# Performance work log

Hardware: AMD Instinct MI355X
Metric: run time of the kernel (lower is better)

## Reference

```python
import jax, jax.numpy as jnp
import numpy as np

B, NQ, C = 2, 16384, 768
NH, NL, NP = 6, 1, 4
HW = 128
D = C // NH  # 128, deform_ratio = 1.0
EPS = 1e-6


def layernorm(x, g, b):
    m = jnp.mean(x, -1, keepdims=True)
    v = jnp.var(x, -1, keepdims=True)
    return (x - m) * jax.lax.rsqrt(v + EPS) * g + b


def setup_inputs() -> dict:
    key = jax.random.key(0)
    ks = jax.random.split(key, 16)
    n = lambda k, s, sc=1.0: jax.random.normal(k, s, jnp.float32) * sc
    return {
        "query": n(ks[0], (B, NQ, C)),
        "reference_points": jax.random.uniform(ks[1], (B, NQ, NL, 2), jnp.float32),
        "feat": n(ks[2], (B, NQ, C)),
        "spatial_shapes": jnp.array([[HW, HW]], jnp.int32),
        "level_start_index": jnp.array([0], jnp.int32),
        "qn_g": jnp.ones((C,), jnp.float32), "qn_b": jnp.zeros((C,), jnp.float32),
        "fn_g": jnp.ones((C,), jnp.float32), "fn_b": jnp.zeros((C,), jnp.float32),
        "gamma": n(ks[3], (C,), 0.1),
        "W_off": n(ks[4], (C, NH * NL * NP * 2), 0.02), "b_off": n(ks[5], (NH * NL * NP * 2,), 0.5),
        "W_attn": n(ks[6], (C, NH * NL * NP), 0.02), "b_attn": jnp.zeros((NH * NL * NP,), jnp.float32),
        "W_val": n(ks[7], (C, NH * D), 0.02), "b_val": jnp.zeros((NH * D,), jnp.float32),
        "W_out": n(ks[8], (NH * D, C), 0.02), "b_out": jnp.zeros((C,), jnp.float32),
    }


def _ms_deform_attn(q, rp, f, W_off, b_off, W_attn, b_attn, W_val, b_val, W_out, b_out, shapes, starts):
    Bq, Nq, _ = q.shape
    value = (f @ W_val + b_val).reshape(Bq, -1, NH, D)  # (B, Lin, H, D)
    off = (q @ W_off + b_off).reshape(Bq, Nq, NH, NL, NP, 2)
    aw = jax.nn.softmax((q @ W_attn + b_attn).reshape(Bq, Nq, NH, NL * NP), -1)
    aw = aw.reshape(Bq, Nq, NH, NL, NP)
    shapes_f = jnp.asarray(shapes, q.dtype)
    normalizer = jnp.stack([shapes_f[:, 1], shapes_f[:, 0]], -1)  # (NL, 2) = (W, H)
    loc = rp[:, :, None, :, None, :] + off / normalizer[None, None, None, :, None, :]
    out = jnp.zeros((Bq, Nq, NH, D), q.dtype)
    b_idx = jnp.arange(Bq)[:, None, None, None]
    h_idx = jnp.arange(NH)[None, None, :, None]
    for l in range(NL):
        Hl, Wl = int(shapes[l, 0]), int(shapes[l, 1])
        s = int(starts[l])
        v = value[:, s:s + Hl * Wl].reshape(Bq, Hl, Wl, NH, D)
        ll = loc[:, :, :, l]                        # (B, Nq, H, P, 2)
        # grid_sample bilinear, align_corners=False, zero padding
        x = ll[..., 0] * Wl - 0.5
        y = ll[..., 1] * Hl - 0.5
        x0 = jnp.floor(x); y0 = jnp.floor(y)
        x1 = x0 + 1.0;     y1 = y0 + 1.0
        wx1 = x - x0; wx0 = 1.0 - wx1
        wy1 = y - y0; wy0 = 1.0 - wy1
        def corner(xi, yi, w):
            valid = (xi >= 0) & (xi <= Wl - 1) & (yi >= 0) & (yi <= Hl - 1)
            xc = jnp.clip(xi, 0, Wl - 1).astype(jnp.int32)
            yc = jnp.clip(yi, 0, Hl - 1).astype(jnp.int32)
            g = v[b_idx, yc, xc, h_idx]             # (B, Nq, H, P, D)
            return g * (w * valid)[..., None]
        samp = (corner(x0, y0, wx0 * wy0) + corner(x1, y0, wx1 * wy0)
                + corner(x0, y1, wx0 * wy1) + corner(x1, y1, wx1 * wy1))
        out = out + jnp.einsum('bqhpd,bqhp->bqhd', samp, aw[:, :, :, l])
    return out.reshape(Bq, Nq, NH * D) @ W_out + b_out


def reference(query, reference_points, feat, spatial_shapes, level_start_index,
              qn_g, qn_b, fn_g, fn_b, gamma,
              W_off, b_off, W_attn, b_attn, W_val, b_val, W_out, b_out):
    shapes = np.asarray(spatial_shapes)
    starts = np.asarray(level_start_index)
    q = layernorm(query, qn_g, qn_b)
    f = layernorm(feat, fn_g, fn_b)
    attn = _ms_deform_attn(q, reference_points, f, W_off, b_off, W_attn, b_attn,
                           W_val, b_val, W_out, b_out, shapes, starts)
    return query + gamma * attn
```

## Files before the change

kernel.cpp:

```cpp
#include <hip/hip_runtime.h>
#include <stdint.h>

typedef unsigned short u16;
typedef float f32x4 __attribute__((ext_vector_type(4)));
typedef short s16x8 __attribute__((ext_vector_type(8)));

#define K_DIM 768
#define M_ROWS 32768
#define NQ_ 16384
#define HW_ 128

__device__ __forceinline__ float bf2f(u16 u) {
    union { uint32_t u; float f; } c; c.u = ((uint32_t)u) << 16; return c.f;
}
__device__ __forceinline__ u16 f2bf(float f) {
    union { float f; uint32_t u; } c; c.f = f;
    uint32_t u = c.u;
    u += 0x7FFFu + ((u >> 16) & 1);
    return (u16)(u >> 16);
}

__device__ __forceinline__ void gload_lds16(const void* g, void* l) {
    __builtin_amdgcn_global_load_lds((const __attribute__((address_space(1))) void*)g,
                                     (__attribute__((address_space(3))) void*)l, 16, 0, 0);
}

__global__ void prep_all_kernel(const float* __restrict__ Wval, const float* __restrict__ Wout,
                                const float* __restrict__ Woff, const float* __restrict__ Wattn,
                                const float* __restrict__ boff, const float* __restrict__ battn,
                                u16* __restrict__ wv_t, u16* __restrict__ wo_t,
                                u16* __restrict__ woa_t, float* __restrict__ bias) {
    int idx = blockIdx.x * 256 + threadIdx.x;
    const int SZ = 768 * K_DIM;
    if (idx < SZ) {
        int n = idx / K_DIM, k = idx - n * K_DIM;
        wv_t[idx] = f2bf(Wval[(size_t)k * 768 + n]);
    } else if (idx < 2 * SZ) {
        int r = idx - SZ;
        int n = r / K_DIM, k = r - n * K_DIM;
        wo_t[r] = f2bf(Wout[(size_t)k * 768 + n]);
    } else if (idx < 2 * SZ + 128 * K_DIM) {
        int r = idx - 2 * SZ;
        int n = r / K_DIM, k = r - n * K_DIM;
        float v = 0.0f;
        if (n < 48)      v = Woff[(size_t)k * 48 + n];
        else if (n < 72) v = Wattn[(size_t)k * 24 + (n - 48)];
        woa_t[r] = f2bf(v);
        if (r < 128) bias[r] = r < 48 ? boff[r] : (r < 72 ? battn[r - 48] : 0.0f);
    }
}

__global__ __launch_bounds__(192) void ln_kernel(const float* __restrict__ x,
                                                 const float* __restrict__ g,
                                                 const float* __restrict__ b,
                                                 u16* __restrict__ out) {
    int row = blockIdx.x;
    int tid = threadIdx.x;
    const float4 v = ((const float4*)(x + (size_t)row * K_DIM))[tid];
    float s  = v.x + v.y + v.z + v.w;
    float s2 = v.x * v.x + v.y * v.y + v.z * v.z + v.w * v.w;
#pragma unroll
    for (int off = 32; off >= 1; off >>= 1) {
        s  += __shfl_down(s, off);
        s2 += __shfl_down(s2, off);
    }
    __shared__ float red[6];
    int wv = tid >> 6, lane = tid & 63;
    if (lane == 0) { red[wv] = s; red[3 + wv] = s2; }
    __syncthreads();
    s  = red[0] + red[1] + red[2];
    s2 = red[3] + red[4] + red[5];
    float mean = s * (1.0f / K_DIM);
    float var  = s2 * (1.0f / K_DIM) - mean * mean;
    float inv  = rsqrtf(var + 1e-6f);
    const float4 gg = ((const float4*)g)[tid];
    const float4 bb = ((const float4*)b)[tid];
    ushort4 o;
    o.x = f2bf((v.x - mean) * inv * gg.x + bb.x);
    o.y = f2bf((v.y - mean) * inv * gg.y + bb.y);
    o.z = f2bf((v.z - mean) * inv * gg.z + bb.z);
    o.w = f2bf((v.w - mean) * inv * gg.w + bb.w);
    ((ushort4*)(out + (size_t)row * K_DIM))[tid] = o;
}

#define EP_BF16 0
#define EP_F32 1
#define EP_FINAL 2

template <int EP, int NX, int BN = 128>
__global__ __launch_bounds__(512) void gemm_kernel(
        const u16* __restrict__ A, const u16* __restrict__ Bt,
        const float* __restrict__ bias, void* __restrict__ out, int ld_out,
        const float* __restrict__ query, const float* __restrict__ gamma) {
    constexpr int NF = BN / 64;
    constexpr int BCH = BN / 64;
    constexpr int BUF = 16384 + BN * 128;
    constexpr int NWG = NX * (M_ROWS / 128);
    constexpr int CPX = NWG / 8;
    __shared__ __align__(16) char smem[2 * BUF];
    const int lane = threadIdx.x & 63;
    const int wv = threadIdx.x >> 6;
    const int wr = wv >> 2, wc = wv & 3;
    const int lr = lane & 15, lg = lane >> 4;
    const int wg  = blockIdx.x;
    const int swz = (wg & 7) * CPX + (wg >> 3);
    const int m0 = (swz / NX) * 128;
    const int n0 = (swz % NX) * BN;

    f32x4 acc[4][NF] = {};

    const u16* Ab = A + (size_t)m0 * K_DIM;
    const u16* Bb = Bt + (size_t)n0 * K_DIM;

    auto stage = [&](char* buf, int kt) {
#pragma unroll
        for (int c = 0; c < 2; ++c) {
            int chunk = wv * 2 + c;
            int row = chunk * 8 + (lane >> 3);
            int slot = (lane & 7) ^ (row & 7);
            gload_lds16(Ab + (size_t)row * K_DIM + kt + slot * 8, buf + chunk * 1024);
        }
#pragma unroll
        for (int c = 0; c < BCH; ++c) {
            int chunk = wv * BCH + c;
            int row = chunk * 8 + (lane >> 3);
            int slot = (lane & 7) ^ (row & 7);
            gload_lds16(Bb + (size_t)row * K_DIM + kt + slot * 8, buf + 16384 + chunk * 1024);
        }
    };

    stage(smem, 0);
    asm volatile("s_waitcnt vmcnt(0)" ::: "memory");
    __builtin_amdgcn_s_barrier();
    __builtin_amdgcn_sched_barrier(0);

    constexpr int NT = K_DIM / 64;
    int cur = 0;
#pragma unroll 2
    for (int t = 0; t < NT; ++t) {
        const char* rb = smem + cur * BUF;
        if (t + 1 < NT) stage(smem + (cur ^ 1) * BUF, (t + 1) * 64);
#pragma unroll
        for (int kk = 0; kk < 2; ++kk) {
            s16x8 af[4], bfr[NF];
#pragma unroll
            for (int m = 0; m < 4; ++m) {
                int row = wr * 64 + m * 16 + lr;
                int slot = (kk * 4 + lg) ^ (row & 7);
                af[m] = *(const s16x8*)(rb + row * 128 + slot * 16);
            }
#pragma unroll
            for (int n = 0; n < NF; ++n) {
                int row = wc * (BN / 4) + n * 16 + lr;
                int slot = (kk * 4 + lg) ^ (row & 7);
                bfr[n] = *(const s16x8*)(rb + 16384 + row * 128 + slot * 16);
            }
            __builtin_amdgcn_s_setprio(1);
#pragma unroll
            for (int m = 0; m < 4; ++m)
#pragma unroll
                for (int n = 0; n < NF; ++n)
                    acc[m][n] = __builtin_amdgcn_mfma_f32_16x16x32_bf16(af[m], bfr[n], acc[m][n], 0, 0, 0);
            __builtin_amdgcn_s_setprio(0);
        }
        asm volatile("s_waitcnt vmcnt(0)" ::: "memory");
        __builtin_amdgcn_s_barrier();
        __builtin_amdgcn_sched_barrier(0);
        cur ^= 1;
    }

#pragma unroll
    for (int m = 0; m < 4; ++m) {
#pragma unroll
        for (int r = 0; r < 4; ++r) {
            int row = m0 + wr * 64 + m * 16 + lg * 4 + r;
#pragma unroll
            for (int n = 0; n < NF; ++n) {
                int col = n0 + wc * (BN / 4) + n * 16 + lr;
                float v = acc[m][n][r] + bias[col];
                if constexpr (EP == EP_BF16) {
                    ((u16*)out)[(size_t)row * ld_out + col] = f2bf(v);
                } else if constexpr (EP == EP_F32) {
                    if (col < 72)
                        ((float*)out)[(size_t)row * ld_out + col] = v;
                } else {
                    size_t idx = (size_t)row * ld_out + col;
                    ((float*)out)[idx] = query[idx] + gamma[col] * v;
                }
            }
        }
    }
}

__global__ __launch_bounds__(384) void sample_kernel(
        const float* __restrict__ oa,
        const float* __restrict__ rp,
        const u16* __restrict__ value,
        u16* __restrict__ samp) {
    const int q = blockIdx.x;
    const int h = __builtin_amdgcn_readfirstlane(threadIdx.x >> 6);
    const int lane = threadIdx.x & 63;
    const int b = q >> 14;
    const float* oar = oa + (size_t)q * 128;

    const int p  = (lane >> 2) & 3;
    const int cn = lane & 3;
    const float lp = oar[48 + h * 4 + p];
    const float e  = __expf(lp);
    float es = e;
    es += __shfl_xor(es, 4);
    es += __shfl_xor(es, 8);
    const float aw = e * __builtin_amdgcn_rcpf(es);

    const float2 offv = *(const float2*)(oar + h * 8 + p * 2);
    const float2 rpv  = *(const float2*)(rp + (size_t)q * 2);
    const float xx = rpv.x * 128.0f + offv.x - 0.5f;
    const float yy = rpv.y * 128.0f + offv.y - 0.5f;
    const float x0 = floorf(xx), y0 = floorf(yy);
    const float fx = xx - x0, fy = yy - y0;
    const float cx = x0 + (float)(cn & 1);
    const float cy = y0 + (float)(cn >> 1);
    const float wx = (cn & 1) ? fx : 1.0f - fx;
    const float wy = (cn >> 1) ? fy : 1.0f - fy;
    const bool valid = (cx >= 0.0f) & (cx <= 127.0f) & (cy >= 0.0f) & (cy <= 127.0f);
    const float w = valid ? aw * wx * wy : 0.0f;
    const int cxi = (int)fminf(fmaxf(cx, 0.0f), 127.0f);
    const int cyi = (int)fminf(fmaxf(cy, 0.0f), 127.0f);
    const int packed = (__float_as_int(w) & 0xffff0000) | (cyi * HW_ + cxi);

    const char* vbs = (const char*)value + 2u * ((size_t)b * NQ_ * K_DIM + (size_t)h * 128);
    float acc0 = 0.0f, acc1 = 0.0f;
#pragma unroll
    for (int c = 0; c < 16; ++c) {
        const int pc = __builtin_amdgcn_readlane(packed, c);
        const float wc = __int_as_float(pc & 0xffff0000);
        const int   oc = (pc & 0xffff) * (K_DIM * 2);
        const uint32_t d = ((const uint32_t*)(vbs + oc))[lane];
        acc0 = fmaf(wc, __int_as_float(d << 16), acc0);
        acc1 = fmaf(wc, __int_as_float(d), acc1);
    }
    ushort2 o; o.x = f2bf(acc0); o.y = f2bf(acc1);
    ((ushort2*)(samp + (size_t)q * K_DIM + h * 128))[lane] = o;
}

extern "C" void kernel_launch(void* const* d_in, const int* in_sizes, int n_in,
                              void* d_out, int out_size, void* d_ws, size_t ws_size,
                              hipStream_t stream) {
    (void)in_sizes; (void)n_in; (void)out_size; (void)ws_size;
    const float* query  = (const float*)d_in[0];
    const float* rp     = (const float*)d_in[1];
    const float* feat   = (const float*)d_in[2];
    const float* qn_g   = (const float*)d_in[5];
    const float* qn_b   = (const float*)d_in[6];
    const float* fn_g   = (const float*)d_in[7];
    const float* fn_b   = (const float*)d_in[8];
    const float* gamma  = (const float*)d_in[9];
    const float* W_off  = (const float*)d_in[10];
    const float* b_off  = (const float*)d_in[11];
    const float* W_attn = (const float*)d_in[12];
    const float* b_attn = (const float*)d_in[13];
    const float* W_val  = (const float*)d_in[14];
    const float* b_val  = (const float*)d_in[15];
    const float* W_out  = (const float*)d_in[16];
    const float* b_out  = (const float*)d_in[17];

    char* ws = (char*)d_ws;
    u16*   ln_buf  = (u16*)  (ws + 0);
    u16*   val_buf = (u16*)  (ws + 50331648);
    float* oa_buf  = (float*)(ws + 100663296);
    u16*   wv_t    = (u16*)  (ws + 117440512);
    u16*   wo_t    = (u16*)  (ws + 118620160);
    u16*   woa_t   = (u16*)  (ws + 119799808);
    float* bias_oa = (float*)(ws + 119996416);
    u16*   samp_buf = ln_buf;

    prep_all_kernel<<<(2 * 768 * 768 + 128 * 768 + 255) / 256, 256, 0, stream>>>(
        W_val, W_out, W_off, W_attn, b_off, b_attn, wv_t, wo_t, woa_t, bias_oa);

    ln_kernel<<<M_ROWS, 192, 0, stream>>>(feat, fn_g, fn_b, ln_buf);

    gemm_kernel<EP_BF16, 6><<<6 * (M_ROWS / 128), 512, 0, stream>>>(ln_buf, wv_t, b_val, val_buf, 768, nullptr, nullptr);

    ln_kernel<<<M_ROWS, 192, 0, stream>>>(query, qn_g, qn_b, ln_buf);

    gemm_kernel<EP_F32, 2, 64><<<2 * (M_ROWS / 128), 512, 0, stream>>>(ln_buf, woa_t, bias_oa, oa_buf, 128, nullptr, nullptr);

    sample_kernel<<<M_ROWS, 384, 0, stream>>>(oa_buf, rp, val_buf, samp_buf);

    gemm_kernel<EP_FINAL, 6><<<6 * (M_ROWS / 128), 512, 0, stream>>>(samp_buf, wo_t, b_out, d_out, 768, query, gamma);
}
```

Measured before the change: 264.3 us.

## Store value and offset/attention buffers head-major; sample per head across queries

The value GEMM epilogue now writes a head-major layout of 128-element bf16 rows (256 bytes) per head, and the offset/attention GEMM writes a compact per-head 12-float record. The sample kernel is regridded so each block handles one head for 8 consecutive queries rather than all heads of one query. Each head's 128x128 value plane stays contiguous (4 MB per batch), which is meant to improve cache locality of the random gathers. The trade-off is scattered, less coalesced stores in the GEMM epilogues.

New measurement: 246.8 us. -6.6%, faster.

```diff
diff --git a/kernel.cpp b/kernel.cpp
--- a/kernel.cpp
+++ b/kernel.cpp
@@ -83,8 +83,8 @@
     ((ushort4*)(out + (size_t)row * K_DIM))[tid] = o;
 }
 
-#define EP_BF16 0
-#define EP_F32 1
+#define EP_VAL 0
+#define EP_OA 1
 #define EP_FINAL 2
 
 template <int EP, int NX, int BN = 128>
@@ -178,11 +178,15 @@
             for (int n = 0; n < NF; ++n) {
                 int col = n0 + wc * (BN / 4) + n * 16 + lr;
                 float v = acc[m][n][r] + bias[col];
-                if constexpr (EP == EP_BF16) {
-                    ((u16*)out)[(size_t)row * ld_out + col] = f2bf(v);
-                } else if constexpr (EP == EP_F32) {
-                    if (col < 72)
-                        ((float*)out)[(size_t)row * ld_out + col] = v;
+                if constexpr (EP == EP_VAL) {
+                    ((u16*)out)[((size_t)(col >> 7) * M_ROWS + row) * 128 + (col & 127)] = f2bf(v);
+                } else if constexpr (EP == EP_OA) {
+                    if (col < 72) {
+                        int hh, s;
+                        if (col < 48) { hh = col >> 3; s = col & 7; }
+                        else          { hh = (col - 48) >> 2; s = 8 + ((col - 48) & 3); }
+                        ((float*)out)[((size_t)hh * M_ROWS + row) * 12 + s] = v;
+                    }
                 } else {
                     size_t idx = (size_t)row * ld_out + col;
                     ((float*)out)[idx] = query[idx] + gamma[col] * v;
@@ -192,27 +196,28 @@
     }
 }
 
-__global__ __launch_bounds__(384) void sample_kernel(
-        const float* __restrict__ oa,
+__global__ __launch_bounds__(512) void sample_kernel(
+        const float* __restrict__ oa2,
         const float* __restrict__ rp,
         const u16* __restrict__ value,
         u16* __restrict__ samp) {
-    const int q = blockIdx.x;
-    const int h = __builtin_amdgcn_readfirstlane(threadIdx.x >> 6);
+    const int h = blockIdx.x >> 12;
+    const int q = __builtin_amdgcn_readfirstlane(
+                      ((blockIdx.x & 4095) << 3) + (threadIdx.x >> 6));
     const int lane = threadIdx.x & 63;
     const int b = q >> 14;
-    const float* oar = oa + (size_t)q * 128;
+    const float* oar = oa2 + ((size_t)h * M_ROWS + q) * 12;
 
     const int p  = (lane >> 2) & 3;
     const int cn = lane & 3;
-    const float lp = oar[48 + h * 4 + p];
+    const float lp = oar[8 + p];
     const float e  = __expf(lp);
     float es = e;
     es += __shfl_xor(es, 4);
     es += __shfl_xor(es, 8);
     const float aw = e * __builtin_amdgcn_rcpf(es);
 
-    const float2 offv = *(const float2*)(oar + h * 8 + p * 2);
+    const float2 offv = *(const float2*)(oar + p * 2);
     const float2 rpv  = *(const float2*)(rp + (size_t)q * 2);
     const float xx = rpv.x * 128.0f + offv.x - 0.5f;
     const float yy = rpv.y * 128.0f + offv.y - 0.5f;
@@ -228,13 +233,13 @@
     const int cyi = (int)fminf(fmaxf(cy, 0.0f), 127.0f);
     const int packed = (__float_as_int(w) & 0xffff0000) | (cyi * HW_ + cxi);
 
-    const char* vbs = (const char*)value + 2u * ((size_t)b * NQ_ * K_DIM + (size_t)h * 128);
+    const char* vbs = (const char*)value + ((size_t)h * M_ROWS + (size_t)b * NQ_) * 256;
     float acc0 = 0.0f, acc1 = 0.0f;
 #pragma unroll
     for (int c = 0; c < 16; ++c) {
         const int pc = __builtin_amdgcn_readlane(packed, c);
         const float wc = __int_as_float(pc & 0xffff0000);
-        const int   oc = (pc & 0xffff) * (K_DIM * 2);
+        const int   oc = (pc & 0x3fff) << 8;
         const uint32_t d = ((const uint32_t*)(vbs + oc))[lane];
         acc0 = fmaf(wc, __int_as_float(d << 16), acc0);
         acc1 = fmaf(wc, __int_as_float(d), acc1);
@@ -267,7 +272,7 @@
     char* ws = (char*)d_ws;
     u16*   ln_buf  = (u16*)  (ws + 0);
     u16*   val_buf = (u16*)  (ws + 50331648);
-    float* oa_buf  = (float*)(ws + 100663296);
+    float* oa2_buf = (float*)(ws + 100663296);
     u16*   wv_t    = (u16*)  (ws + 117440512);
     u16*   wo_t    = (u16*)  (ws + 118620160);
     u16*   woa_t   = (u16*)  (ws + 119799808);
@@ -279,13 +284,13 @@
 
     ln_kernel<<<M_ROWS, 192, 0, stream>>>(feat, fn_g, fn_b, ln_buf);
 
-    gemm_kernel<EP_BF16, 6><<<6 * (M_ROWS / 128), 512, 0, stream>>>(ln_buf, wv_t, b_val, val_buf, 768, nullptr, nullptr);
+    gemm_kernel<EP_VAL, 6><<<6 * (M_ROWS / 128), 512, 0, stream>>>(ln_buf, wv_t, b_val, val_buf, 768, nullptr, nullptr);
 
     ln_kernel<<<M_ROWS, 192, 0, stream>>>(query, qn_g, qn_b, ln_buf);
 
-    gemm_kernel<EP_F32, 2, 64><<<2 * (M_ROWS / 128), 512, 0, stream>>>(ln_buf, woa_t, bias_oa, oa_buf, 128, nullptr, nullptr);
-
-    sample_kernel<<<M_ROWS, 384, 0, stream>>>(oa_buf, rp, val_buf, samp_buf);
+    gemm_kernel<EP_OA, 2, 64><<<2 * (M_ROWS / 128), 512, 0, stream>>>(ln_buf, woa_t, bias_oa, oa2_buf, 0, nullptr, nullptr);
+
+    sample_kernel<<<6 * 4096, 512, 0, stream>>>(oa2_buf, rp, val_buf, samp_buf);
 
     gemm_kernel<EP_FINAL, 6><<<6 * (M_ROWS / 128), 512, 0, stream>>>(samp_buf, wo_t, b_out, d_out, 768, query, gamma);
 }
```
